# Performance work log

Hardware: AMD Instinct MI355X
Metric: run time of the kernel (lower is better)

## Reference

```python
import jax, jax.numpy as jnp
import numpy as np

FEAT_STRIDE = 16
SCALES = (8.0, 16.0, 32.0)
RATIOS = (0.5, 1.0, 2.0)
NEG_TH = 0.3
POS_TH = 0.7
FG_FRACTION = 0.5
RPN_BATCHSIZE = 256
A = 9  # num anchors per location


def generate_anchors(base_size=16, ratios=RATIOS, scales=SCALES):
    """Standard py-faster-rcnn anchor generation (ratio-major, scale-minor)."""
    base = np.array([0.0, 0.0, base_size - 1.0, base_size - 1.0])
    w = base[2] - base[0] + 1.0
    h = base[3] - base[1] + 1.0
    xc = base[0] + 0.5 * (w - 1.0)
    yc = base[1] + 0.5 * (h - 1.0)
    ratios = np.asarray(ratios, dtype=np.float64)
    scales = np.asarray(scales, dtype=np.float64)
    size = w * h
    ws = np.round(np.sqrt(size / ratios))          # [3]
    hs = np.round(ws * ratios)                     # [3]
    ws = (ws[:, None] * scales[None, :]).reshape(-1)  # [9]
    hs = (hs[:, None] * scales[None, :]).reshape(-1)
    anchors = np.stack([xc - 0.5 * (ws - 1.0), yc - 0.5 * (hs - 1.0),
                        xc + 0.5 * (ws - 1.0), yc + 0.5 * (hs - 1.0)], axis=1)
    return anchors.astype(np.float32)  # [9,4]


def _rank_desc(scores, mask):
    """Rank (0 = largest) of each element among masked entries, per row."""
    s = jnp.where(mask, scores, -jnp.inf)
    order = jnp.argsort(-s, axis=1)
    return jnp.argsort(order, axis=1)


def setup_inputs() -> dict:
    key = jax.random.key(0)
    k1, k2, k3, k4, k5, k6 = jax.random.split(key, 6)
    B, K, H, W = 32, 50, 64, 64
    IMG = float(H * FEAT_STRIDE)  # 1024
    rpn_cls_score = jax.random.normal(k1, (B, 2 * A, H, W), dtype=jnp.float32)
    x1 = jax.random.uniform(k2, (B, K)) * (IMG - 220.0)
    y1 = jax.random.uniform(k3, (B, K)) * (IMG - 220.0)
    bw = jax.random.uniform(k4, (B, K)) * 180.0 + 16.0
    bh = jax.random.uniform(k5, (B, K)) * 180.0 + 16.0
    gt_boxes = jnp.stack([x1, y1, x1 + bw, y1 + bh, jnp.ones((B, K))], axis=-1).astype(jnp.float32)
    im_info = jnp.tile(jnp.array([[IMG, IMG, 1.0]], dtype=jnp.float32), (B, 1))
    num_boxes = jax.random.randint(k6, (B,), 1, K + 1).astype(jnp.int32)
    return {"rpn_cls_score": rpn_cls_score, "gt_boxes": gt_boxes,
            "im_info": im_info, "num_boxes": num_boxes}


def reference(rpn_cls_score, gt_boxes, im_info, num_boxes):
    B = gt_boxes.shape[0]
    K = gt_boxes.shape[1]
    H, W = rpn_cls_score.shape[2], rpn_cls_score.shape[3]

    anchors = jnp.asarray(generate_anchors())  # [A,4]
    sx = jnp.arange(W, dtype=jnp.float32) * FEAT_STRIDE
    sy = jnp.arange(H, dtype=jnp.float32) * FEAT_STRIDE
    gx, gy = jnp.meshgrid(sx, sy)  # [H,W]
    shifts = jnp.stack([gx.ravel(), gy.ravel(), gx.ravel(), gy.ravel()], axis=1)  # [HW,4]
    all_anchors = (anchors[None, :, :] + shifts[:, None, :]).reshape(-1, 4)  # [N,4], N=HW*A
    N = all_anchors.shape[0]

    im_h, im_w = im_info[0, 0], im_info[0, 1]
    inside = ((all_anchors[:, 0] >= 0) & (all_anchors[:, 1] >= 0) &
              (all_anchors[:, 2] < im_w) & (all_anchors[:, 3] < im_h))  # [N]

    # pairwise IoU [B,N,K] with +1 pixel convention
    gt4 = gt_boxes[..., :4]
    ax1, ay1, ax2, ay2 = (all_anchors[None, :, None, i] for i in range(4))
    gx1, gy1, gx2, gy2 = (gt4[:, None, :, i] for i in range(4))
    iw = jnp.maximum(jnp.minimum(ax2, gx2) - jnp.maximum(ax1, gx1) + 1.0, 0.0)
    ih = jnp.maximum(jnp.minimum(ay2, gy2) - jnp.maximum(ay1, gy1) + 1.0, 0.0)
    inter = iw * ih
    a_area = ((all_anchors[:, 2] - all_anchors[:, 0] + 1.0) *
              (all_anchors[:, 3] - all_anchors[:, 1] + 1.0))[None, :, None]
    g_area = ((gt4[..., 2] - gt4[..., 0] + 1.0) * (gt4[..., 3] - gt4[..., 1] + 1.0))[:, None, :]
    ov = inter / (a_area + g_area - inter)
    valid = (jnp.arange(K)[None, :] < num_boxes[:, None])  # [B,K]
    ov = jnp.where(valid[:, None, :], ov, -1.0)

    max_ov = ov.max(axis=2)       # [B,N]
    argmax = ov.argmax(axis=2)    # [B,N]
    gt_max = ov.max(axis=1)       # [B,K]
    gt_max = jnp.where(gt_max == 0.0, 1e-5, gt_max)
    best = ((ov == gt_max[:, None, :]) & valid[:, None, :]).any(axis=2)  # [B,N]

    lab = jnp.full((B, N), -1.0, dtype=jnp.float32)
    lab = jnp.where(inside[None, :] & (max_ov < NEG_TH), 0.0, lab)
    lab = jnp.where(inside[None, :] & best, 1.0, lab)
    lab = jnp.where(inside[None, :] & (max_ov >= POS_TH), 1.0, lab)

    # random subsampling of positives / negatives
    skey = jax.random.key(42)
    kf, kb = jax.random.split(skey)
    num_fg = int(FG_FRACTION * RPN_BATCHSIZE)
    fg_mask = lab == 1.0
    rk_fg = _rank_desc(jax.random.uniform(kf, (B, N)), fg_mask)
    lab = jnp.where(fg_mask & (rk_fg >= num_fg), -1.0, lab)
    fg_cnt = (lab == 1.0).sum(axis=1)
    num_bg = RPN_BATCHSIZE - fg_cnt  # [B]
    bg_mask = lab == 0.0
    rk_bg = _rank_desc(jax.random.uniform(kb, (B, N)), bg_mask)
    lab = jnp.where(bg_mask & (rk_bg >= num_bg[:, None]), -1.0, lab)

    assigned = jnp.take_along_axis(gt4, argmax[:, :, None], axis=1)  # [B,N,4]
    ew = all_anchors[:, 2] - all_anchors[:, 0] + 1.0
    eh = all_anchors[:, 3] - all_anchors[:, 1] + 1.0
    ecx = all_anchors[:, 0] + 0.5 * ew
    ecy = all_anchors[:, 1] + 0.5 * eh
    gw = assigned[..., 2] - assigned[..., 0] + 1.0
    gh = assigned[..., 3] - assigned[..., 1] + 1.0
    gcx = assigned[..., 0] + 0.5 * gw
    gcy = assigned[..., 1] + 0.5 * gh
    tgt = jnp.stack([(gcx - ecx[None]) / ew[None], (gcy - ecy[None]) / eh[None],
                     jnp.log(gw / ew[None]), jnp.log(gh / eh[None])], axis=-1)  # [B,N,4]
    tgt = jnp.where(inside[None, :, None], tgt, 0.0)

    in_w = jnp.where((lab == 1.0)[:, :, None], 1.0, 0.0) * jnp.ones((4,), jnp.float32)
    num_examples = (lab >= 0.0).sum(axis=1).astype(jnp.float32)  # [B]
    out_w = jnp.where((lab >= 0.0)[:, :, None], (1.0 / num_examples)[:, None, None], 0.0) \
            * jnp.ones((4,), jnp.float32)

    labels_out = lab.reshape(B, H, W, A).transpose(0, 3, 1, 2).reshape(B, 1, A * H, W)
    tgt_out = tgt.reshape(B, H, W, A * 4).transpose(0, 3, 1, 2)
    in_w_out = in_w.reshape(B, H, W, A * 4).transpose(0, 3, 1, 2)
    out_w_out = out_w.reshape(B, H, W, A * 4).transpose(0, 3, 1, 2)
    return (labels_out, tgt_out, in_w_out, out_w_out)
```

## Files before the change

### kernel.cpp

```cpp
#include <hip/hip_runtime.h>
#include <stdint.h>

#pragma clang fp contract(off)

#define NBATCH 32
#define NK 50
#define NH 64
#define NW 64
#define NA 9
#define NN (NH * NW * NA)
#define BN (NBATCH * NN)
#define HWSZ (NH * NW)

constexpr size_t OFF_AMAX  = 0;
constexpr size_t OFF_PK    = OFF_AMAX + (size_t)BN * 4;
constexpr size_t OFF_GTMAX = OFF_PK + (size_t)BN * 4;
constexpr size_t OFF_NUMEX = OFF_GTMAX + (size_t)NBATCH * NK * 4;
constexpr size_t OFF_THR   = OFF_NUMEX + (size_t)NBATCH * 4;

constexpr size_t OUT_LAB  = 0;
constexpr size_t OUT_TGT  = (size_t)NBATCH * NA * HWSZ;
constexpr size_t OUT_INW  = OUT_TGT + (size_t)NBATCH * NA * 4 * HWSZ;
constexpr size_t OUT_OUTW = OUT_INW + (size_t)NBATCH * NA * 4 * HWSZ;

__constant__ float c_anch[NA][4] = {
    {-84.f, -40.f, 99.f, 55.f},    {-176.f, -88.f, 191.f, 103.f},
    {-360.f, -184.f, 375.f, 199.f}, {-56.f, -56.f, 71.f, 71.f},
    {-120.f, -120.f, 135.f, 135.f}, {-248.f, -248.f, 263.f, 263.f},
    {-36.f, -80.f, 51.f, 95.f},    {-80.f, -168.f, 95.f, 183.f},
    {-168.f, -344.f, 183.f, 359.f}};

struct TF2 { uint32_t a, b; };

__host__ __device__ constexpr uint32_t rotl32(uint32_t x, int d) {
  return (x << d) | (x >> (32 - d));
}

__host__ __device__ constexpr TF2 threefry2x32(uint32_t k0, uint32_t k1,
                                               uint32_t x0, uint32_t x1) {
  uint32_t ks2 = k0 ^ k1 ^ 0x1BD11BDAu;
  x0 += k0; x1 += k1;
  x0 += x1; x1 = rotl32(x1, 13); x1 ^= x0;
  x0 += x1; x1 = rotl32(x1, 15); x1 ^= x0;
  x0 += x1; x1 = rotl32(x1, 26); x1 ^= x0;
  x0 += x1; x1 = rotl32(x1, 6);  x1 ^= x0;
  x0 += k1; x1 += ks2 + 1u;
  x0 += x1; x1 = rotl32(x1, 17); x1 ^= x0;
  x0 += x1; x1 = rotl32(x1, 29); x1 ^= x0;
  x0 += x1; x1 = rotl32(x1, 16); x1 ^= x0;
  x0 += x1; x1 = rotl32(x1, 24); x1 ^= x0;
  x0 += ks2; x1 += k0 + 2u;
  x0 += x1; x1 = rotl32(x1, 13); x1 ^= x0;
  x0 += x1; x1 = rotl32(x1, 15); x1 ^= x0;
  x0 += x1; x1 = rotl32(x1, 26); x1 ^= x0;
  x0 += x1; x1 = rotl32(x1, 6);  x1 ^= x0;
  x0 += k0; x1 += k1 + 3u;
  x0 += x1; x1 = rotl32(x1, 17); x1 ^= x0;
  x0 += x1; x1 = rotl32(x1, 29); x1 ^= x0;
  x0 += x1; x1 = rotl32(x1, 16); x1 ^= x0;
  x0 += x1; x1 = rotl32(x1, 24); x1 ^= x0;
  x0 += k1; x1 += ks2 + 4u;
  x0 += x1; x1 = rotl32(x1, 13); x1 ^= x0;
  x0 += x1; x1 = rotl32(x1, 15); x1 ^= x0;
  x0 += x1; x1 = rotl32(x1, 26); x1 ^= x0;
  x0 += x1; x1 = rotl32(x1, 6);  x1 ^= x0;
  x0 += ks2; x1 += k0 + 5u;
  return TF2{x0, x1};
}

constexpr TF2 KEY_FG = threefry2x32(0u, 42u, 0u, 0u);
constexpr TF2 KEY_BG = threefry2x32(0u, 42u, 0u, 1u);

__device__ inline uint32_t rand23(uint32_t k0, uint32_t k1, uint32_t idx) {
  TF2 r = threefry2x32(k0, k1, 0u, idx);
  return (r.a ^ r.b) >> 9;
}

__device__ inline float iou1(float ax1, float ay1, float ax2, float ay2,
                             float gx1, float gy1, float gx2, float gy2) {
  float iw = fminf(ax2, gx2) - fmaxf(ax1, gx1) + 1.0f;
  iw = fmaxf(iw, 0.0f);
  float ih = fminf(ay2, gy2) - fmaxf(ay1, gy1) + 1.0f;
  ih = fmaxf(ih, 0.0f);
  float inter = iw * ih;
  float aa = (ax2 - ax1 + 1.0f) * (ay2 - ay1 + 1.0f);
  float ga = (gx2 - gx1 + 1.0f) * (gy2 - gy1 + 1.0f);
  return inter / (aa + ga - inter);
}

__global__ __launch_bounds__(256) void k_gtmax(const float* __restrict__ gt,
                                               const int* __restrict__ nbox,
                                               float* __restrict__ gtmax) {
  int b = blockIdx.x / NK;
  int k = blockIdx.x % NK;
  if (k >= nbox[b]) {
    if (threadIdx.x == 0) gtmax[blockIdx.x] = -1.0f;
    return;
  }
  const float* g = gt + ((size_t)b * NK + k) * 5;
  float gx1 = g[0], gy1 = g[1], gx2 = g[2], gy2 = g[3];
  float m = 0.0f;
#pragma unroll
  for (int a = 0; a < NA; ++a) {
    float bx1 = c_anch[a][0], by1 = c_anch[a][1];
    float bx2 = c_anch[a][2], by2 = c_anch[a][3];
    int ix_lo = max(0, (int)floorf((gx1 - 1.0f - bx2) * 0.0625f) - 1);
    int ix_hi = min(NW - 1, (int)ceilf((gx2 + 1.0f - bx1) * 0.0625f) + 1);
    int iy_lo = max(0, (int)floorf((gy1 - 1.0f - by2) * 0.0625f) - 1);
    int iy_hi = min(NH - 1, (int)ceilf((gy2 + 1.0f - by1) * 0.0625f) + 1);
    if (ix_lo > ix_hi || iy_lo > iy_hi) continue;
    int nx = ix_hi - ix_lo + 1;
    int ny = iy_hi - iy_lo + 1;
    int lg = 32 - __clz(nx - 1);
    int tot = ny << lg;
    unsigned mask = (1u << lg) - 1u;
    for (int c = threadIdx.x; c < tot; c += 256) {
      int ixo = c & mask;
      if (ixo >= nx) continue;
      int ix = ix_lo + ixo;
      int iy = iy_lo + (c >> lg);
      float sx = (float)(ix * 16), sy = (float)(iy * 16);
      m = fmaxf(m, iou1(bx1 + sx, by1 + sy, bx2 + sx, by2 + sy, gx1, gy1, gx2, gy2));
    }
  }
  for (int o = 1; o < 64; o <<= 1) m = fmaxf(m, __shfl_xor(m, o));
  __shared__ float ws4[4];
  if ((threadIdx.x & 63) == 0) ws4[threadIdx.x >> 6] = m;
  __syncthreads();
  if (threadIdx.x == 0) {
    m = fmaxf(fmaxf(ws4[0], ws4[1]), fmaxf(ws4[2], ws4[3]));
    if (m == 0.0f) m = 1e-5f;
    gtmax[blockIdx.x] = m;
  }
}

__global__ __launch_bounds__(256) void k_label(const float* __restrict__ gt,
                                               const int* __restrict__ nbox,
                                               const float* __restrict__ gtmax,
                                               const float* __restrict__ iminfo,
                                               unsigned* __restrict__ pk2,
                                               int* __restrict__ amax2) {
  int bid = blockIdx.x;
  int b = bid / (NA * 16);
  int rem = bid - b * (NA * 16);
  int a = rem >> 4;
  int cell0 = (rem & 15) << 8;
  float bx1 = c_anch[a][0], by1 = c_anch[a][1];
  float bx2 = c_anch[a][2], by2 = c_anch[a][3];
  int tid = threadIdx.x;

  __shared__ float cx1[NK], cy1[NK], cx2[NK], cy2[NK], cga[NK], cgm[NK];
  __shared__ int ckk[NK];
  __shared__ int cN;
  if (tid < 64) {
    int m = nbox[b];
    bool keep = false;
    float gx1 = 0, gy1 = 0, gx2 = 0, gy2 = 0, gm = 0;
    if (tid < m) {
      const float* g = gt + ((size_t)b * NK + tid) * 5;
      gx1 = g[0]; gy1 = g[1]; gx2 = g[2]; gy2 = g[3];
      gm = gtmax[b * NK + tid];
      float sy0 = (float)((cell0 >> 6) << 4);
      float lo = fmaxf(by1 + sy0, gy1);
      float hi = fminf(by2 + sy0 + 48.0f, gy2);
      keep = (hi - lo + 2.0f) > 0.0f;
    }
    unsigned long long mk = __ballot(keep);
    if (keep) {
      int pos = (int)__popcll(mk & ((1ull << tid) - 1ull));
      cx1[pos] = gx1; cy1[pos] = gy1; cx2[pos] = gx2; cy2[pos] = gy2;
      cga[pos] = (gx2 - gx1 + 1.0f) * (gy2 - gy1 + 1.0f);
      cgm[pos] = gm; ckk[pos] = tid;
    }
    if (tid == 0) cN = (int)__popcll(mk);
  }
  __syncthreads();

  int cell = cell0 + tid;
  float sx = (float)((cell & 63) << 4);
  float sy = (float)((cell >> 6) << 4);
  float ax1 = bx1 + sx, ay1 = by1 + sy;
  float ax2 = bx2 + sx, ay2 = by2 + sy;
  float aa = (bx2 - bx1 + 1.0f) * (by2 - by1 + 1.0f);
  float best = 0.0f;
  int bi = 0;
  bool isbest = false;
  int M = cN;
  for (int j = 0; j < M; ++j) {
    float iw = fminf(ax2, cx2[j]) - fmaxf(ax1, cx1[j]) + 1.0f;
    iw = fmaxf(iw, 0.0f);
    float ih = fminf(ay2, cy2[j]) - fmaxf(ay1, cy1[j]) + 1.0f;
    ih = fmaxf(ih, 0.0f);
    float inter = iw * ih;
    float ov = inter / (aa + cga[j] - inter);
    if (ov > best) { best = ov; bi = ckk[j]; }
    isbest |= (ov == cgm[j]);
  }
  float imh = iminfo[0], imw = iminfo[1];
  bool inside = (ax1 >= 0.0f) && (ay1 >= 0.0f) && (ax2 < imw) && (ay2 < imh);
  int lab = -1;
  if (inside) {
    if (best < 0.3f) lab = 0;
    if (isbest) lab = 1;
    if (best >= 0.7f) lab = 1;
  }
  int n = cell * NA + a;
  uint32_t kk0 = (lab == 1) ? KEY_FG.a : KEY_BG.a;
  uint32_t kk1 = (lab == 1) ? KEY_FG.b : KEY_BG.b;
  uint32_t v = rand23(kk0, kk1, (uint32_t)(b * NN + n));
  int tp = b * NN + a * HWSZ + cell;
  pk2[tp] = (v << 2) | (uint32_t)(lab + 1);
  amax2[tp] = bi;
}

__global__ __launch_bounds__(1024) void k_select(const unsigned* __restrict__ pk2,
                                                 float* __restrict__ numex,
                                                 uint4* __restrict__ thr) {
  int b = blockIdx.x;
  int base_lab = b * NN;
  int tid = threadIdx.x;

  __shared__ unsigned hF[4096];
  __shared__ unsigned hB[4096];
  __shared__ unsigned listV[2][1024];
  __shared__ unsigned listI[2][1024];
  __shared__ unsigned waveTot[4];
  __shared__ int sFG, sBG, sCross, sBs[2], sR1[2];
  __shared__ unsigned sCnt[2];
  __shared__ unsigned sV[2], sI[2];
  for (int i = tid; i < 4096; i += 1024) { hF[i] = 0; hB[i] = 0; }
  if (tid == 0) { sFG = 0; sBG = 0; sCnt[0] = 0; sCnt[1] = 0; }
  __syncthreads();

  const uint4* pk4 = (const uint4*)(pk2 + base_lab);

  int cfg = 0, cbg = 0;
  for (int i = tid; i < NN / 4; i += 1024) {
    uint4 P4 = pk4[i];
    unsigned pks[4] = {P4.x, P4.y, P4.z, P4.w};
#pragma unroll
    for (int j = 0; j < 4; ++j) {
      unsigned code = pks[j] & 3u;
      cfg += (code == 2u);
      cbg += (code == 1u);
      if (code == 2u) atomicAdd(&hF[pks[j] >> 13], 1u);
      else if (code == 1u) atomicAdd(&hB[pks[j] >> 13], 1u);
    }
  }
  for (int o = 1; o < 64; o <<= 1) { cfg += __shfl_xor(cfg, o); cbg += __shfl_xor(cbg, o); }
  if ((tid & 63) == 0) { atomicAdd(&sFG, cfg); atomicAdd(&sBG, cbg); }
  __syncthreads();

  int fg = sFG, bg = sBG;
  int fgk = min(fg, 128);
  int Cf = 128;
  int Cb = 256 - fgk;
  if (tid == 0) numex[b] = (float)(fgk + min(bg, Cb));
  bool actF = fg > Cf;
  bool actB = bg > Cb;
  if (!actF && !actB) {
    if (tid == 0) thr[b] = make_uint4(0u, 0x7FFFFFFFu, 0u, 0x7FFFFFFFu);
    return;
  }

  for (int cls = 0; cls < 2; ++cls) {
    bool act = (cls == 0) ? actF : actB;
    if (!act) continue;
    const unsigned* h = (cls == 0) ? hF : hB;
    unsigned C = (unsigned)((cls == 0) ? Cf : Cb);
    if (tid == 0) sCross = -1;
    __syncthreads();
    unsigned myChunk = 0, suf = 0;
    if (tid < 256) {
      for (int j = 0; j < 16; ++j) myChunk += h[tid * 16 + j];
      unsigned ss = myChunk;
      int lane = tid & 63;
#pragma unroll
      for (int o = 1; o < 64; o <<= 1) {
        unsigned t2 = __shfl_down(ss, o);
        if (lane + o < 64) ss += t2;
      }
      suf = ss;
      if (lane == 0) waveTot[tid >> 6] = ss;
    }
    __syncthreads();
    if (tid < 256) {
      int w = tid >> 6;
      for (int w2 = w + 1; w2 < 4; ++w2) suf += waveTot[w2];
      if (suf >= C) atomicMax(&sCross, tid);
    }
    __syncthreads();
    if (tid == sCross) {
      unsigned cum = suf - myChunk;
      int i = tid * 16 + 15;
      for (;; --i) {
        unsigned c = h[i];
        if (cum + c >= C) break;
        cum += c;
      }
      sBs[cls] = i; sR1[cls] = (int)(C - cum);
    }
    __syncthreads();
  }

  int BsF = actF ? sBs[0] : -1;
  int BsB = actB ? sBs[1] : -1;
  for (int i = tid; i < NN / 4; i += 1024) {
    uint4 P4 = pk4[i];
    unsigned pks[4] = {P4.x, P4.y, P4.z, P4.w};
#pragma unroll
    for (int j = 0; j < 4; ++j) {
      unsigned code = pks[j] & 3u;
      int bk = (int)(pks[j] >> 13);
      int cls = -1;
      if (code == 2u && bk == BsF) cls = 0;
      else if (code == 1u && bk == BsB) cls = 1;
      if (cls >= 0) {
        int f = 4 * i + j;
        unsigned n = (unsigned)((f & 4095) * NA + (f >> 12));
        unsigned p = atomicAdd(&sCnt[cls], 1u);
        if (p < 1024u) { listV[cls][p] = pks[j] >> 2; listI[cls][p] = n; }
      }
    }
  }
  __syncthreads();

  for (int cls = 0; cls < 2; ++cls) {
    bool act = (cls == 0) ? actF : actB;
    if (!act) continue;
    unsigned L = min(sCnt[cls], 1024u);
    unsigned target = (unsigned)(sR1[cls] - 1);
    for (unsigned i = tid; i < L; i += 1024) {
      unsigned vi = listV[cls][i], xi = listI[cls][i];
      unsigned rank = 0;
      for (unsigned j = 0; j < L; ++j) {
        unsigned vj = listV[cls][j], xj = listI[cls][j];
        rank += (vj > vi) || (vj == vi && xj < xi);
      }
      if (rank == target) { sV[cls] = vi; sI[cls] = xi; }
    }
  }
  __syncthreads();
  if (tid == 0) {
    uint4 t;
    t.x = actF ? sV[0] : 0u;  t.y = actF ? sI[0] : 0x7FFFFFFFu;
    t.z = actB ? sV[1] : 0u;  t.w = actB ? sI[1] : 0x7FFFFFFFu;
    thr[b] = t;
  }
}

__global__ __launch_bounds__(256) void k_out(const float* __restrict__ gt,
                                             const unsigned* __restrict__ pk2,
                                             const int* __restrict__ amax2,
                                             const float* __restrict__ iminfo,
                                             const float* __restrict__ numex,
                                             const uint4* __restrict__ thr,
                                             float* __restrict__ out) {
  int q = blockIdx.x * 256 + threadIdx.x;
  if (q >= (int)(OUT_TGT / 4)) return;
  int xx4 = q & 15;
  int yy = (q >> 4) & 63;
  int ba = q >> 10;
  int a = ba % NA;
  int b = ba / NA;
  int xx0 = xx4 * 4;
  int yx0 = yy * NW + xx0;

  float imh = iminfo[0], imw = iminfo[1];
  float inv_ne = 1.0f / numex[b];
  uint4 th = thr[b];

  int t4 = ba * HWSZ + yx0;
  uint4 pkq = *(const uint4*)(pk2 + t4);
  int4 amq = *(const int4*)(amax2 + t4);
  unsigned pkv[4] = {pkq.x, pkq.y, pkq.z, pkq.w};
  int amv[4] = {amq.x, amq.y, amq.z, amq.w};

  float bx1 = c_anch[a][0], by1 = c_anch[a][1];
  float bx2 = c_anch[a][2], by2 = c_anch[a][3];
  float sy = (float)(yy * 16);

  float labf[4], iwv[4], owv[4], tg[4][4];
#pragma unroll
  for (int u = 0; u < 4; ++u) {
    int xx = xx0 + u;
    int n = (yy * NW + xx) * NA + a;
    unsigned pk = pkv[u];
    int lab = (int)(pk & 3u) - 1;
    if (lab >= 0) {
      unsigned v = pk >> 2;
      unsigned vs = (lab == 1) ? th.x : th.z;
      unsigned is = (lab == 1) ? th.y : th.w;
      bool keep = (v > vs) || (v == vs && (unsigned)n <= is);
      if (!keep) lab = -1;
    }
    labf[u] = (float)lab;
    float sx = (float)(xx * 16);
    float ax1 = bx1 + sx, ay1 = by1 + sy, ax2 = bx2 + sx, ay2 = by2 + sy;
    bool inside = (ax1 >= 0.0f) && (ay1 >= 0.0f) && (ax2 < imw) && (ay2 < imh);
    float t0 = 0.f, t1 = 0.f, t2 = 0.f, t3 = 0.f;
    if (inside) {
      const float* g = gt + ((size_t)b * NK + amv[u]) * 5;
      float ew = ax2 - ax1 + 1.0f, eh = ay2 - ay1 + 1.0f;
      float ecx = ax1 + 0.5f * ew, ecy = ay1 + 0.5f * eh;
      float gw = g[2] - g[0] + 1.0f, gh = g[3] - g[1] + 1.0f;
      float gcx = g[0] + 0.5f * gw, gcy = g[1] + 0.5f * gh;
      t0 = (gcx - ecx) / ew;
      t1 = (gcy - ecy) / eh;
      t2 = logf(gw / ew);
      t3 = logf(gh / eh);
    }
    tg[0][u] = t0; tg[1][u] = t1; tg[2][u] = t2; tg[3][u] = t3;
    iwv[u] = (lab == 1) ? 1.0f : 0.0f;
    owv[u] = (lab >= 0) ? inv_ne : 0.0f;
  }

  *(float4*)(out + OUT_LAB + (size_t)ba * HWSZ + yx0) =
      make_float4(labf[0], labf[1], labf[2], labf[3]);
  size_t tb = OUT_TGT + ((size_t)b * NA * 4 + a * 4) * HWSZ + yx0;
#pragma unroll
  for (int d = 0; d < 4; ++d)
    *(float4*)(out + tb + (size_t)d * HWSZ) =
        make_float4(tg[d][0], tg[d][1], tg[d][2], tg[d][3]);
  size_t ib = OUT_INW + ((size_t)b * NA * 4 + a * 4) * HWSZ + yx0;
  float4 iw4 = make_float4(iwv[0], iwv[1], iwv[2], iwv[3]);
#pragma unroll
  for (int d = 0; d < 4; ++d) *(float4*)(out + ib + (size_t)d * HWSZ) = iw4;
  size_t ob = OUT_OUTW + ((size_t)b * NA * 4 + a * 4) * HWSZ + yx0;
  float4 ow4 = make_float4(owv[0], owv[1], owv[2], owv[3]);
#pragma unroll
  for (int d = 0; d < 4; ++d) *(float4*)(out + ob + (size_t)d * HWSZ) = ow4;
}

extern "C" void kernel_launch(void* const* d_in, const int* in_sizes, int n_in,
                              void* d_out, int out_size, void* d_ws, size_t ws_size,
                              hipStream_t stream) {
  (void)in_sizes; (void)n_in; (void)out_size; (void)ws_size;
  const float* gt     = (const float*)d_in[1];
  const float* iminfo = (const float*)d_in[2];
  const int*   nbox   = (const int*)d_in[3];
  float* out = (float*)d_out;
  char* ws = (char*)d_ws;

  int*      amax2 = (int*)(ws + OFF_AMAX);
  unsigned* pk2   = (unsigned*)(ws + OFF_PK);
  float*    gtmax = (float*)(ws + OFF_GTMAX);
  float*    numex = (float*)(ws + OFF_NUMEX);
  uint4*    thr   = (uint4*)(ws + OFF_THR);

  k_gtmax<<<NBATCH * NK, 256, 0, stream>>>(gt, nbox, gtmax);
  k_label<<<NBATCH * NA * 16, 256, 0, stream>>>(gt, nbox, gtmax, iminfo, pk2, amax2);
  k_select<<<NBATCH, 1024, 0, stream>>>(pk2, numex, thr);
  k_out<<<(int)(OUT_TGT / 4 / 256), 256, 0, stream>>>(gt, pk2, amax2, iminfo, numex, thr, out);
}
```

Baseline: 145.2 us.

## Pack argmax gt index into label word and interleave batch across blocks

```diff
diff --git a/kernel.cpp b/kernel.cpp
--- a/kernel.cpp
+++ b/kernel.cpp
@@ -12,8 +12,7 @@
 #define BN (NBATCH * NN)
 #define HWSZ (NH * NW)
 
-constexpr size_t OFF_AMAX  = 0;
-constexpr size_t OFF_PK    = OFF_AMAX + (size_t)BN * 4;
+constexpr size_t OFF_PK    = 0;
 constexpr size_t OFF_GTMAX = OFF_PK + (size_t)BN * 4;
 constexpr size_t OFF_NUMEX = OFF_GTMAX + (size_t)NBATCH * NK * 4;
 constexpr size_t OFF_THR   = OFF_NUMEX + (size_t)NBATCH * 4;
@@ -91,13 +90,14 @@
 __global__ __launch_bounds__(256) void k_gtmax(const float* __restrict__ gt,
                                                const int* __restrict__ nbox,
                                                float* __restrict__ gtmax) {
-  int b = blockIdx.x / NK;
-  int k = blockIdx.x % NK;
+  int b = blockIdx.x & 31;
+  int k = blockIdx.x >> 5;
+  int gi = b * NK + k;
   if (k >= nbox[b]) {
-    if (threadIdx.x == 0) gtmax[blockIdx.x] = -1.0f;
+    if (threadIdx.x == 0) gtmax[gi] = -1.0f;
     return;
   }
-  const float* g = gt + ((size_t)b * NK + k) * 5;
+  const float* g = gt + (size_t)gi * 5;
   float gx1 = g[0], gy1 = g[1], gx2 = g[2], gy2 = g[3];
   float m = 0.0f;
 #pragma unroll
@@ -130,7 +130,7 @@
   if (threadIdx.x == 0) {
     m = fmaxf(fmaxf(ws4[0], ws4[1]), fmaxf(ws4[2], ws4[3]));
     if (m == 0.0f) m = 1e-5f;
-    gtmax[blockIdx.x] = m;
+    gtmax[gi] = m;
   }
 }
 
@@ -138,13 +138,11 @@
                                                const int* __restrict__ nbox,
                                                const float* __restrict__ gtmax,
                                                const float* __restrict__ iminfo,
-                                               unsigned* __restrict__ pk2,
-                                               int* __restrict__ amax2) {
-  int bid = blockIdx.x;
-  int b = bid / (NA * 16);
-  int rem = bid - b * (NA * 16);
-  int a = rem >> 4;
-  int cell0 = (rem & 15) << 8;
+                                               unsigned* __restrict__ pk2) {
+  int b = blockIdx.x & 31;
+  int j = blockIdx.x >> 5;
+  int a = j >> 4;
+  int cell0 = (j & 15) << 8;
   float bx1 = c_anch[a][0], by1 = c_anch[a][1];
   float bx2 = c_anch[a][2], by2 = c_anch[a][3];
   int tid = threadIdx.x;
@@ -186,15 +184,15 @@
   int bi = 0;
   bool isbest = false;
   int M = cN;
-  for (int j = 0; j < M; ++j) {
-    float iw = fminf(ax2, cx2[j]) - fmaxf(ax1, cx1[j]) + 1.0f;
+  for (int j2 = 0; j2 < M; ++j2) {
+    float iw = fminf(ax2, cx2[j2]) - fmaxf(ax1, cx1[j2]) + 1.0f;
     iw = fmaxf(iw, 0.0f);
-    float ih = fminf(ay2, cy2[j]) - fmaxf(ay1, cy1[j]) + 1.0f;
+    float ih = fminf(ay2, cy2[j2]) - fmaxf(ay1, cy1[j2]) + 1.0f;
     ih = fmaxf(ih, 0.0f);
     float inter = iw * ih;
-    float ov = inter / (aa + cga[j] - inter);
-    if (ov > best) { best = ov; bi = ckk[j]; }
-    isbest |= (ov == cgm[j]);
+    float ov = inter / (aa + cga[j2] - inter);
+    if (ov > best) { best = ov; bi = ckk[j2]; }
+    isbest |= (ov == cgm[j2]);
   }
   float imh = iminfo[0], imw = iminfo[1];
   bool inside = (ax1 >= 0.0f) && (ay1 >= 0.0f) && (ax2 < imw) && (ay2 < imh);
@@ -208,9 +206,8 @@
   uint32_t kk0 = (lab == 1) ? KEY_FG.a : KEY_BG.a;
   uint32_t kk1 = (lab == 1) ? KEY_FG.b : KEY_BG.b;
   uint32_t v = rand23(kk0, kk1, (uint32_t)(b * NN + n));
-  int tp = b * NN + a * HWSZ + cell;
-  pk2[tp] = (v << 2) | (uint32_t)(lab + 1);
-  amax2[tp] = bi;
+  pk2[b * NN + a * HWSZ + cell] =
+      (v << 8) | ((uint32_t)bi << 2) | (uint32_t)(lab + 1);
 }
 
 __global__ __launch_bounds__(1024) void k_select(const unsigned* __restrict__ pk2,
@@ -243,8 +240,8 @@
       unsigned code = pks[j] & 3u;
       cfg += (code == 2u);
       cbg += (code == 1u);
-      if (code == 2u) atomicAdd(&hF[pks[j] >> 13], 1u);
-      else if (code == 1u) atomicAdd(&hB[pks[j] >> 13], 1u);
+      if (code == 2u) atomicAdd(&hF[pks[j] >> 19], 1u);
+      else if (code == 1u) atomicAdd(&hB[pks[j] >> 19], 1u);
     }
   }
   for (int o = 1; o < 64; o <<= 1) { cfg += __shfl_xor(cfg, o); cbg += __shfl_xor(cbg, o); }
@@ -311,7 +308,7 @@
 #pragma unroll
     for (int j = 0; j < 4; ++j) {
       unsigned code = pks[j] & 3u;
-      int bk = (int)(pks[j] >> 13);
+      int bk = (int)(pks[j] >> 19);
       int cls = -1;
       if (code == 2u && bk == BsF) cls = 0;
       else if (code == 1u && bk == BsB) cls = 1;
@@ -319,7 +316,7 @@
         int f = 4 * i + j;
         unsigned n = (unsigned)((f & 4095) * NA + (f >> 12));
         unsigned p = atomicAdd(&sCnt[cls], 1u);
-        if (p < 1024u) { listV[cls][p] = pks[j] >> 2; listI[cls][p] = n; }
+        if (p < 1024u) { listV[cls][p] = pks[j] >> 8; listI[cls][p] = n; }
       }
     }
   }
@@ -351,19 +348,18 @@
 
 __global__ __launch_bounds__(256) void k_out(const float* __restrict__ gt,
                                              const unsigned* __restrict__ pk2,
-                                             const int* __restrict__ amax2,
                                              const float* __restrict__ iminfo,
                                              const float* __restrict__ numex,
                                              const uint4* __restrict__ thr,
                                              float* __restrict__ out) {
-  int q = blockIdx.x * 256 + threadIdx.x;
-  if (q >= (int)(OUT_TGT / 4)) return;
-  int xx4 = q & 15;
-  int yy = (q >> 4) & 63;
-  int ba = q >> 10;
-  int a = ba % NA;
-  int b = ba / NA;
-  int xx0 = xx4 * 4;
+  int b = blockIdx.x & 31;
+  int j = blockIdx.x >> 5;
+  int a = j >> 2;
+  int yq = j & 3;
+  int tid = threadIdx.x;
+  int yy = (yq << 4) + (tid >> 4);
+  int xx0 = (tid & 15) << 2;
+  int ba = b * NA + a;
   int yx0 = yy * NW + xx0;
 
   float imh = iminfo[0], imw = iminfo[1];
@@ -372,9 +368,7 @@
 
   int t4 = ba * HWSZ + yx0;
   uint4 pkq = *(const uint4*)(pk2 + t4);
-  int4 amq = *(const int4*)(amax2 + t4);
   unsigned pkv[4] = {pkq.x, pkq.y, pkq.z, pkq.w};
-  int amv[4] = {amq.x, amq.y, amq.z, amq.w};
 
   float bx1 = c_anch[a][0], by1 = c_anch[a][1];
   float bx2 = c_anch[a][2], by2 = c_anch[a][3];
@@ -388,7 +382,7 @@
     unsigned pk = pkv[u];
     int lab = (int)(pk & 3u) - 1;
     if (lab >= 0) {
-      unsigned v = pk >> 2;
+      unsigned v = pk >> 8;
       unsigned vs = (lab == 1) ? th.x : th.z;
       unsigned is = (lab == 1) ? th.y : th.w;
       bool keep = (v > vs) || (v == vs && (unsigned)n <= is);
@@ -400,7 +394,8 @@
     bool inside = (ax1 >= 0.0f) && (ay1 >= 0.0f) && (ax2 < imw) && (ay2 < imh);
     float t0 = 0.f, t1 = 0.f, t2 = 0.f, t3 = 0.f;
     if (inside) {
-      const float* g = gt + ((size_t)b * NK + amv[u]) * 5;
+      int am = (int)((pk >> 2) & 63u);
+      const float* g = gt + ((size_t)b * NK + am) * 5;
       float ew = ax2 - ax1 + 1.0f, eh = ay2 - ay1 + 1.0f;
       float ecx = ax1 + 0.5f * ew, ecy = ay1 + 0.5f * eh;
       float gw = g[2] - g[0] + 1.0f, gh = g[3] - g[1] + 1.0f;
@@ -442,14 +437,13 @@
   float* out = (float*)d_out;
   char* ws = (char*)d_ws;
 
-  int*      amax2 = (int*)(ws + OFF_AMAX);
   unsigned* pk2   = (unsigned*)(ws + OFF_PK);
   float*    gtmax = (float*)(ws + OFF_GTMAX);
   float*    numex = (float*)(ws + OFF_NUMEX);
   uint4*    thr   = (uint4*)(ws + OFF_THR);
 
-  k_gtmax<<<NBATCH * NK, 256, 0, stream>>>(gt, nbox, gtmax);
-  k_label<<<NBATCH * NA * 16, 256, 0, stream>>>(gt, nbox, gtmax, iminfo, pk2, amax2);
+  k_gtmax<<<NK * NBATCH, 256, 0, stream>>>(gt, nbox, gtmax);
+  k_label<<<144 * NBATCH, 256, 0, stream>>>(gt, nbox, gtmax, iminfo, pk2);
   k_select<<<NBATCH, 1024, 0, stream>>>(pk2, numex, thr);
-  k_out<<<(int)(OUT_TGT / 4 / 256), 256, 0, stream>>>(gt, pk2, amax2, iminfo, numex, thr, out);
-}
+  k_out<<<36 * NBATCH, 256, 0, stream>>>(gt, pk2, iminfo, numex, thr, out);
+}
```

New measurement: 146.4 us. No clear change (+0.8%).
